# Performance work log

Hardware: AMD Instinct MI355X
Metric: run time of the kernel (lower is better)

Reference implementation:

```python
import jax, jax.numpy as jnp
import numpy as np

N = 100000
F_IN = 128
H = 64
E = 3200000


def setup_inputs() -> dict:
    key = jax.random.key(0)
    ks = jax.random.split(key, 10)
    x = jax.random.normal(ks[0], (N, F_IN), dtype=jnp.float32)
    edge_index = jax.random.randint(ks[1], (2, E), 0, N, dtype=jnp.int64)
    hidden_state = jax.random.normal(ks[2], (1, N, H), dtype=jnp.float32)
    # GCNConv params (glorot-ish scale)
    W_gcn = jax.random.normal(ks[3], (F_IN, H), dtype=jnp.float32) / np.sqrt(F_IN)
    b_gcn = jnp.zeros((H,), dtype=jnp.float32)
    # torch.nn.GRU params, layout [3H, in] with gate order (r, z, n)
    s = 1.0 / np.sqrt(H)
    W_ih = jax.random.uniform(ks[4], (3 * H, H), dtype=jnp.float32, minval=-s, maxval=s)
    W_hh = jax.random.uniform(ks[5], (3 * H, H), dtype=jnp.float32, minval=-s, maxval=s)
    b_ih = jax.random.uniform(ks[6], (3 * H,), dtype=jnp.float32, minval=-s, maxval=s)
    b_hh = jax.random.uniform(ks[7], (3 * H,), dtype=jnp.float32, minval=-s, maxval=s)
    return {"x": x, "edge_index": edge_index, "hidden_state": hidden_state,
            "W_gcn": W_gcn, "b_gcn": b_gcn,
            "W_ih": W_ih, "W_hh": W_hh, "b_ih": b_ih, "b_hh": b_hh}


def gcn_conv(x, edge_index, W, b):
    n = x.shape[0]
    # add self-loops (PyG GCNConv default)
    loops = jnp.arange(n, dtype=edge_index.dtype)
    row = jnp.concatenate([edge_index[0], loops])  # source
    col = jnp.concatenate([edge_index[1], loops])  # target
    # symmetric normalization: deg over targets with unit edge weights
    deg = jax.ops.segment_sum(jnp.ones_like(col, dtype=x.dtype), col, num_segments=n)
    dis = jnp.where(deg > 0, jax.lax.rsqrt(deg), 0.0)
    norm = dis[row] * dis[col]  # (E+N,)
    xt = x @ W  # (N, H) transform first, then aggregate
    msg = norm[:, None] * xt[row]  # (E+N, H)
    out = jax.ops.segment_sum(msg, col, num_segments=n)
    return out + b


def gru_step(x, h, W_ih, W_hh, b_ih, b_hh):
    # single-step torch GRU, gate order (r, z, n)
    gi = x @ W_ih.T + b_ih  # (N, 3H)
    gh = h @ W_hh.T + b_hh
    i_r, i_z, i_n = jnp.split(gi, 3, axis=-1)
    h_r, h_z, h_n = jnp.split(gh, 3, axis=-1)
    r = jax.nn.sigmoid(i_r + h_r)
    z = jax.nn.sigmoid(i_z + h_z)
    n = jnp.tanh(i_n + r * h_n)
    return (1.0 - z) * n + z * h


def reference(x, edge_index, hidden_state, W_gcn, b_gcn, W_ih, W_hh, b_ih, b_hh):
    g = jax.nn.relu(gcn_conv(x, edge_index, W_gcn, b_gcn))  # (N, H)
    h_new = gru_step(g, hidden_state[0], W_ih, W_hh, b_ih, b_hh)  # (N, H)
    return h_new, h_new[None]  # (out, new_hidden_state)
```

## Files before the change

kernel.cpp:

```cpp
#include <hip/hip_runtime.h>
#include <cmath>

constexpr int NN  = 100000;
constexpr int FIN = 128;
constexpr int HH  = 64;
constexpr int NE  = 3200000;
constexpr int NB  = (NN + 255) / 256;
constexpr int NFB  = NB;
constexpr int PCAP = 10240;

typedef __attribute__((ext_vector_type(8))) short short8;
typedef __attribute__((ext_vector_type(4))) float f32x4;

__device__ __forceinline__ ushort f2bf(float x) {
    unsigned u = __float_as_uint(x);
    u += 0x7FFF + ((u >> 16) & 1);
    return (ushort)(u >> 16);
}
__device__ __forceinline__ float bf2f(ushort h) {
    return __uint_as_float(((unsigned)h) << 16);
}
__device__ __forceinline__ unsigned pack2(float a, float b) {
    return (unsigned)f2bf(a) | ((unsigned)f2bf(b) << 16);
}

__global__ void __launch_bounds__(256) k_part(const int* __restrict__ ei,
                                              int* __restrict__ gcnt,
                                              int* __restrict__ pairs) {
    __shared__ int lcnt[NFB];
    __shared__ int lbase[NFB];
    int t = threadIdx.x;
    for (int i = t; i < NFB; i += 256) lcnt[i] = 0;
    __syncthreads();

    long long base = (long long)blockIdx.x * 8192;
    int4 r4[8], c4[8];
    int nv[8];
#pragma unroll
    for (int s = 0; s < 8; ++s) {
        long long e = base + s * 1024 + t * 4;
        if (e < NE) {
            r4[s] = ((const int4*)(ei))[e >> 2];
            c4[s] = ((const int4*)(ei + NE))[e >> 2];
            nv[s] = 1;
            atomicAdd(&lcnt[c4[s].x >> 8], 1);
            atomicAdd(&lcnt[c4[s].y >> 8], 1);
            atomicAdd(&lcnt[c4[s].z >> 8], 1);
            atomicAdd(&lcnt[c4[s].w >> 8], 1);
        } else {
            nv[s] = 0;
        }
    }
    __syncthreads();
    for (int i = t; i < NFB; i += 256) {
        int c = lcnt[i];
        lbase[i] = c ? atomicAdd(&gcnt[i], c) : 0;
        lcnt[i] = 0;
    }
    __syncthreads();
#pragma unroll
    for (int s = 0; s < 8; ++s) {
        if (!nv[s]) continue;
        int rr[4] = {r4[s].x, r4[s].y, r4[s].z, r4[s].w};
        int cc[4] = {c4[s].x, c4[s].y, c4[s].z, c4[s].w};
#pragma unroll
        for (int k = 0; k < 4; ++k) {
            int b   = cc[k] >> 8;
            int p   = atomicAdd(&lcnt[b], 1);
            int pos = lbase[b] + p;
            if (pos < PCAP) pairs[(long long)b * PCAP + pos] = (rr[k] << 8) | (cc[k] & 255);
        }
    }
}

__global__ void __launch_bounds__(256) k_csr(const int* __restrict__ pairs,
                                             const int* __restrict__ gcnt,
                                             int* __restrict__ deg,
                                             int* __restrict__ rowptr,
                                             float* __restrict__ dis,
                                             int* __restrict__ csr) {
    __shared__ int sg[256];
    __shared__ int ldeg[256];
    __shared__ int lrp[256];
    __shared__ int lcur[256];
    __shared__ int lcsr[PCAP];
    int f = blockIdx.x;
    int t = threadIdx.x;
    int partial = 0;
    if (t < f) partial += gcnt[t];
    if (t + 256 < f) partial += gcnt[t + 256];
    sg[t] = partial;
    ldeg[t] = 0;
    __syncthreads();
    for (int off = 128; off > 0; off >>= 1) {
        if (t < off) sg[t] += sg[t + off];
        __syncthreads();
    }
    int base = sg[0];
    int cnt  = min(gcnt[f], PCAP);
    int n0   = f * 256;
    const int* pb = pairs + (long long)f * PCAP;
    for (int i = t; i < cnt; i += 256) atomicAdd(&ldeg[pb[i] & 255], 1);
    __syncthreads();
    int v = ldeg[t];
    lrp[t] = v;
    __syncthreads();
    for (int off = 1; off < 256; off <<= 1) {
        int add = (t >= off) ? lrp[t - off] : 0;
        __syncthreads();
        lrp[t] += add;
        __syncthreads();
    }
    int excl = lrp[t] - v;
    if (n0 + t < NN) {
        deg[n0 + t]    = v;
        rowptr[n0 + t] = base + excl;
        dis[n0 + t]    = rsqrtf((float)(v + 1));
    }
    lcur[t] = excl;
    __syncthreads();
    for (int i = t; i < cnt; i += 256) {
        int e = pb[i];
        int p = atomicAdd(&lcur[e & 255], 1);
        lcsr[p] = e >> 8;
    }
    __syncthreads();
    for (int i = t; i < cnt; i += 256) csr[base + i] = lcsr[i];
}

__global__ void __launch_bounds__(256) k_xt(const float* __restrict__ x,
                                            const float* __restrict__ W,
                                            ushort* __restrict__ xtb) {
    __shared__ float part[16 * 256];
    int t    = threadIdx.x;
    int lane = t & 63;
    int kbase = __builtin_amdgcn_readfirstlane((t >> 6) * 32);
    float wreg[32];
#pragma unroll
    for (int kk = 0; kk < 32; ++kk) wreg[kk] = W[(kbase + kk) * HH + lane];

    for (int ph = blockIdx.x; ph < 6250; ph += gridDim.x) {
        int rowBase = ph * 16;
#pragma unroll 2
        for (int r = 0; r < 16; ++r) {
            const float* xr = x + (size_t)(rowBase + r) * FIN + kbase;
            float acc = 0.f;
#pragma unroll
            for (int kk = 0; kk < 32; ++kk) acc = fmaf(xr[kk], wreg[kk], acc);
            part[r * 256 + (kbase << 1) + lane] = acc;
        }
        __syncthreads();
        unsigned* xo = (unsigned*)(xtb + (size_t)rowBase * HH);
        const float2* p2 = (const float2*)part;
#pragma unroll
        for (int rr = 0; rr < 2; ++rr) {
            int u  = t + 256 * rr;
            int r  = u >> 5;
            int cp = u & 31;
            float2 a0 = p2[r * 128 + cp];
            float2 a1 = p2[r * 128 + cp + 32];
            float2 a2 = p2[r * 128 + cp + 64];
            float2 a3 = p2[r * 128 + cp + 96];
            xo[u] = pack2(a0.x + a1.x + a2.x + a3.x, a0.y + a1.y + a2.y + a3.y);
        }
        __syncthreads();
    }
}

__global__ void __launch_bounds__(256) k_gather(const int* __restrict__ csr,
                                                const int* __restrict__ rowptr,
                                                const int* __restrict__ deg,
                                                const float* __restrict__ dis,
                                                const ushort* __restrict__ xtb,
                                                const float* __restrict__ bg,
                                                float* __restrict__ g) {
    __shared__ int   lid[4][64];
    __shared__ float ldi[4][64];
    int t    = threadIdx.x;
    int lane = t & 63;
    int w    = t >> 6;
    int n    = blockIdx.x * 4 + w;
    int r = lane >> 3;
    int q = lane & 7;
    float acc[8] = {0.f, 0.f, 0.f, 0.f, 0.f, 0.f, 0.f, 0.f};
    float dn  = dis[n];
    int start = rowptr[n];
    int cnt   = deg[n];
    for (int c0 = 0; c0 < cnt; c0 += 64) {
        int m = min(64, cnt - c0);
        if (lane < m) {
            int id = csr[start + c0 + lane];
            lid[w][lane] = id;
            ldi[w][lane] = dis[id];
        }
        for (int i = r; i < m; i += 8) {
            int   src = lid[w][i];
            float d   = ldi[w][i];
            short8 v = ((const short8*)(xtb + (size_t)src * HH))[q];
#pragma unroll
            for (int j = 0; j < 8; ++j)
                acc[j] = fmaf(d, bf2f((ushort)v[j]), acc[j]);
        }
    }
#pragma unroll
    for (int j = 0; j < 8; ++j) {
        acc[j] += __shfl_xor(acc[j], 8, 64);
        acc[j] += __shfl_xor(acc[j], 16, 64);
        acc[j] += __shfl_xor(acc[j], 32, 64);
    }
    if (r == 0) {
        short8 xs = ((const short8*)(xtb + (size_t)n * HH))[q];
        float4 b0 = ((const float4*)bg)[q * 2];
        float4 b1 = ((const float4*)bg)[q * 2 + 1];
        float bb[8] = {b0.x, b0.y, b0.z, b0.w, b1.x, b1.y, b1.z, b1.w};
        float res[8];
#pragma unroll
        for (int j = 0; j < 8; ++j)
            res[j] = fmaxf(fmaf(dn, fmaf(dn, bf2f((ushort)xs[j]), acc[j]), bb[j]), 0.f);
        float4* go = (float4*)(g + (size_t)n * HH + q * 8);
        go[0] = make_float4(res[0], res[1], res[2], res[3]);
        go[1] = make_float4(res[4], res[5], res[6], res[7]);
    }
}

__global__ void k_wprep(const float* __restrict__ Wih, const float* __restrict__ Whh,
                        ushort* __restrict__ bsp) {
    ushort* Bhi  = bsp;
    ushort* Blo  = bsp + 192 * 128;
    ushort* BShi = bsp + 2 * 192 * 128;
    ushort* BSlo = BShi + 64 * 64;
    int i = blockIdx.x * 256 + threadIdx.x;
    if (i < 192 * 128) {
        int j = i >> 7, k = i & 127;
        float wv = (k < 64) ? Wih[j * 64 + k] : Whh[j * 64 + (k - 64)];
        ushort hi = f2bf(wv);
        Bhi[i] = hi;
        Blo[i] = f2bf(wv - bf2f(hi));
    }
    if (i < 64 * 64) {
        int j = i >> 6, k = i & 63;
        float wv = Whh[(128 + j) * 64 + k];
        ushort hi = f2bf(wv);
        BShi[i] = hi;
        BSlo[i] = f2bf(wv - bf2f(hi));
    }
}

__global__ void __launch_bounds__(256) k_gru(
    const float* __restrict__ gbuf, const float* __restrict__ hprev,
    const ushort* __restrict__ bsp,
    const float* __restrict__ bih, const float* __restrict__ bhh,
    float* __restrict__ out) {
    __shared__ ushort Ahi[64 * 136];
    __shared__ ushort Alo[64 * 136];
    const ushort* Bhi  = bsp;
    const ushort* Blo  = bsp + 192 * 128;
    const ushort* BShi = bsp + 2 * 192 * 128;
    const ushort* BSlo = BShi + 64 * 64;

    int t  = threadIdx.x;
    int n0 = blockIdx.x * 64;

    unsigned* Ahi32 = (unsigned*)Ahi;
    unsigned* Alo32 = (unsigned*)Alo;
#pragma unroll
    for (int s = 0; s < 4; ++s) {
        int idx = t + 256 * s;
        int nd  = idx >> 4;
        int kq  = idx & 15;
        bool ok = (n0 + nd) < NN;
        float4 vg = ok ? ((const float4*)(gbuf  + (size_t)(n0 + nd) * HH))[kq]
                       : make_float4(0.f, 0.f, 0.f, 0.f);
        float4 vh = ok ? ((const float4*)(hprev + (size_t)(n0 + nd) * HH))[kq]
                       : make_float4(0.f, 0.f, 0.f, 0.f);
        int bg2 = nd * 68 + kq * 2;
        int bh2 = bg2 + 32;
        float ghx = bf2f(f2bf(vg.x)), ghy = bf2f(f2bf(vg.y));
        float ghz = bf2f(f2bf(vg.z)), ghw = bf2f(f2bf(vg.w));
        float hhx = bf2f(f2bf(vh.x)), hhy = bf2f(f2bf(vh.y));
        float hhz = bf2f(f2bf(vh.z)), hhw = bf2f(f2bf(vh.w));
        Ahi32[bg2]     = pack2(vg.x, vg.y);
        Ahi32[bg2 + 1] = pack2(vg.z, vg.w);
        Alo32[bg2]     = pack2(vg.x - ghx, vg.y - ghy);
        Alo32[bg2 + 1] = pack2(vg.z - ghz, vg.w - ghw);
        Ahi32[bh2]     = pack2(vh.x, vh.y);
        Ahi32[bh2 + 1] = pack2(vh.z, vh.w);
        Alo32[bh2]     = pack2(vh.x - hhx, vh.y - hhy);
        Alo32[bh2 + 1] = pack2(vh.z - hhz, vh.w - hhw);
    }
    __syncthreads();

    int lane  = t & 63;
    int w     = t >> 6;
    int l15   = lane & 15;
    int kbase = (lane >> 4) * 8;

    f32x4 acc[4][4];
#pragma unroll
    for (int a = 0; a < 4; ++a)
#pragma unroll
        for (int m = 0; m < 4; ++m) acc[a][m] = (f32x4){0.f, 0.f, 0.f, 0.f};

#pragma unroll
    for (int g = 0; g < 3; ++g) {
        int brow = (w + 4 * g) * 16 + l15;
        short8 bh[4], bl[4];
#pragma unroll
        for (int ks = 0; ks < 4; ++ks) {
            bh[ks] = *(const short8*)(Bhi + brow * 128 + ks * 32 + kbase);
            bl[ks] = *(const short8*)(Blo + brow * 128 + ks * 32 + kbase);
        }
#pragma unroll
        for (int mt = 0; mt < 4; ++mt) {
            int abase = (mt * 16 + l15) * 136 + kbase;
#pragma unroll
            for (int ks = 0; ks < 4; ++ks) {
                short8 ah = *(const short8*)&Ahi[abase + ks * 32];
                short8 al = *(const short8*)&Alo[abase + ks * 32];
                acc[g][mt] = __builtin_amdgcn_mfma_f32_16x16x32_bf16(ah, bh[ks], acc[g][mt], 0, 0, 0);
                acc[g][mt] = __builtin_amdgcn_mfma_f32_16x16x32_bf16(al, bh[ks], acc[g][mt], 0, 0, 0);
                acc[g][mt] = __builtin_amdgcn_mfma_f32_16x16x32_bf16(ah, bl[ks], acc[g][mt], 0, 0, 0);
            }
        }
    }
    {
        int brow = w * 16 + l15;
        short8 bh[2], bl[2];
#pragma unroll
        for (int ks = 0; ks < 2; ++ks) {
            bh[ks] = *(const short8*)(BShi + brow * 64 + ks * 32 + kbase);
            bl[ks] = *(const short8*)(BSlo + brow * 64 + ks * 32 + kbase);
        }
#pragma unroll
        for (int mt = 0; mt < 4; ++mt) {
            int abase = (mt * 16 + l15) * 136 + 64 + kbase;
#pragma unroll
            for (int ks = 0; ks < 2; ++ks) {
                short8 ah = *(const short8*)&Ahi[abase + ks * 32];
                short8 al = *(const short8*)&Alo[abase + ks * 32];
                acc[3][mt] = __builtin_amdgcn_mfma_f32_16x16x32_bf16(ah, bh[ks], acc[3][mt], 0, 0, 0);
                acc[3][mt] = __builtin_amdgcn_mfma_f32_16x16x32_bf16(al, bh[ks], acc[3][mt], 0, 0, 0);
                acc[3][mt] = __builtin_amdgcn_mfma_f32_16x16x32_bf16(ah, bl[ks], acc[3][mt], 0, 0, 0);
            }
        }
    }

    int j = 16 * w + l15;
    float br  = bih[j] + bhh[j];
    float bz  = bih[HH + j] + bhh[HH + j];
    float bin = bih[2 * HH + j];
    float bhn = bhh[2 * HH + j];
#pragma unroll
    for (int mt = 0; mt < 4; ++mt) {
#pragma unroll
        for (int reg = 0; reg < 4; ++reg) {
            int row  = mt * 16 + (lane >> 4) * 4 + reg;
            int node = n0 + row;
            if (node < NN) {
                float S1 = acc[0][mt][reg];
                float S2 = acc[1][mt][reg];
                float S3 = acc[2][mt][reg];
                float Hn = acc[3][mt][reg];
                float r  = __builtin_amdgcn_rcpf(1.f + __expf(-(S1 + br)));
                float z  = __builtin_amdgcn_rcpf(1.f + __expf(-(S2 + bz)));
                float na = (S3 - Hn + bin) + r * (Hn + bhn);
                float e2 = __expf(2.f * na);
                float nv = fmaf(-2.f, __builtin_amdgcn_rcpf(1.f + e2), 1.f);
                int lidx = row * 136 + 64 + j;
                float h  = bf2f(Ahi[lidx]) + bf2f(Alo[lidx]);
                float o  = (1.f - z) * nv + z * h;
                out[(size_t)node * HH + j] = o;
                out[(size_t)NN * HH + (size_t)node * HH + j] = o;
            }
        }
    }
}

extern "C" void kernel_launch(void* const* d_in, const int* in_sizes, int n_in,
                              void* d_out, int out_size, void* d_ws, size_t ws_size,
                              hipStream_t stream) {
    const float* x   = (const float*)d_in[0];
    const int*   ei  = (const int*)d_in[1];
    const float* hs  = (const float*)d_in[2];
    const float* Wg  = (const float*)d_in[3];
    const float* bg  = (const float*)d_in[4];
    const float* Wih = (const float*)d_in[5];
    const float* Whh = (const float*)d_in[6];
    const float* bih = (const float*)d_in[7];
    const float* bhh = (const float*)d_in[8];
    float* out = (float*)d_out;

    char* ws = (char*)d_ws;
    int*    pairs  = (int*)   (ws);
    ushort* xtb    = (ushort*)(ws);
    float*  gbuf   = (float*) (ws + 16400000);
    int*    csr    = (int*)   (ws + 42000000);
    int*    deg    = (int*)   (ws + 54800000);
    int*    rowptr = (int*)   (ws + 55200000);
    float*  dis    = (float*) (ws + 55600000);
    ushort* wsplit = (ushort*)(ws + 56000000);
    int*    gcnt   = (int*)   (ws + 56200000);

    hipMemsetAsync(gcnt, 0, NFB * sizeof(int), stream);

    hipLaunchKernelGGL(k_wprep, dim3(96), dim3(256), 0, stream, Wih, Whh, wsplit);
    hipLaunchKernelGGL(k_part,  dim3((NE + 8191) / 8192), dim3(256), 0, stream, ei, gcnt, pairs);
    hipLaunchKernelGGL(k_csr,   dim3(NFB), dim3(256), 0, stream,
                       pairs, gcnt, deg, rowptr, dis, csr);
    hipLaunchKernelGGL(k_xt,    dim3(1024), dim3(256), 0, stream, x, Wg, xtb);
    hipLaunchKernelGGL(k_gather, dim3(NN / 4), dim3(256), 0, stream,
                       csr, rowptr, deg, dis, xtb, bg, gbuf);
    hipLaunchKernelGGL(k_gru,   dim3((NN + 63) / 64), dim3(256), 0, stream,
                       gbuf, hs, wsplit, bih, bhh, out);
}
```

Measured before the change: 365.1 us.

## Pre-scale transformed features by dis and simplify gather; retune partition and CSR kernels

Folds the source-side degree normalization into the feature transform, so each row of the bf16 xt buffer is already multiplied by dis[src]. This removes the per-edge dis gather and the multiply from the aggregation kernel, which is now unrolled by two to keep more loads in flight. The partition kernel also handles smaller chunks per block, giving more blocks, and the CSR build kernel runs with 512 threads. A small change in bf16 rounding comes from scaling before quantization.

```diff
diff --git a/kernel.cpp b/kernel.cpp
--- a/kernel.cpp
+++ b/kernel.cpp
@@ -8,6 +8,7 @@
 constexpr int NB  = (NN + 255) / 256;
 constexpr int NFB  = NB;
 constexpr int PCAP = 10240;
+constexpr int CH   = 2048;
 
 typedef __attribute__((ext_vector_type(8))) short short8;
 typedef __attribute__((ext_vector_type(4))) float f32x4;
@@ -33,12 +34,12 @@
     for (int i = t; i < NFB; i += 256) lcnt[i] = 0;
     __syncthreads();
 
-    long long base = (long long)blockIdx.x * 8192;
-    int4 r4[8], c4[8];
-    int nv[8];
-#pragma unroll
-    for (int s = 0; s < 8; ++s) {
-        long long e = base + s * 1024 + t * 4;
+    int base = blockIdx.x * CH;
+    int4 r4[2], c4[2];
+    int nv[2];
+#pragma unroll
+    for (int s = 0; s < 2; ++s) {
+        int e = base + s * 1024 + t * 4;
         if (e < NE) {
             r4[s] = ((const int4*)(ei))[e >> 2];
             c4[s] = ((const int4*)(ei + NE))[e >> 2];
@@ -59,7 +60,7 @@
     }
     __syncthreads();
 #pragma unroll
-    for (int s = 0; s < 8; ++s) {
+    for (int s = 0; s < 2; ++s) {
         if (!nv[s]) continue;
         int rr[4] = {r4[s].x, r4[s].y, r4[s].z, r4[s].w};
         int cc[4] = {c4[s].x, c4[s].y, c4[s].z, c4[s].w};
@@ -68,41 +69,38 @@
             int b   = cc[k] >> 8;
             int p   = atomicAdd(&lcnt[b], 1);
             int pos = lbase[b] + p;
-            if (pos < PCAP) pairs[(long long)b * PCAP + pos] = (rr[k] << 8) | (cc[k] & 255);
-        }
-    }
-}
-
-__global__ void __launch_bounds__(256) k_csr(const int* __restrict__ pairs,
+            if (pos < PCAP) pairs[b * PCAP + pos] = (rr[k] << 8) | (cc[k] & 255);
+        }
+    }
+}
+
+__global__ void __launch_bounds__(512) k_csr(const int* __restrict__ pairs,
                                              const int* __restrict__ gcnt,
                                              int* __restrict__ deg,
                                              int* __restrict__ rowptr,
                                              float* __restrict__ dis,
                                              int* __restrict__ csr) {
-    __shared__ int sg[256];
+    __shared__ int sg[512];
     __shared__ int ldeg[256];
-    __shared__ int lrp[256];
+    __shared__ int lrp[512];
     __shared__ int lcur[256];
     __shared__ int lcsr[PCAP];
     int f = blockIdx.x;
     int t = threadIdx.x;
-    int partial = 0;
-    if (t < f) partial += gcnt[t];
-    if (t + 256 < f) partial += gcnt[t + 256];
-    sg[t] = partial;
-    ldeg[t] = 0;
-    __syncthreads();
-    for (int off = 128; off > 0; off >>= 1) {
+    sg[t] = (t < f) ? gcnt[t] : 0;
+    if (t < 256) ldeg[t] = 0;
+    __syncthreads();
+    for (int off = 256; off > 0; off >>= 1) {
         if (t < off) sg[t] += sg[t + off];
         __syncthreads();
     }
     int base = sg[0];
     int cnt  = min(gcnt[f], PCAP);
     int n0   = f * 256;
-    const int* pb = pairs + (long long)f * PCAP;
-    for (int i = t; i < cnt; i += 256) atomicAdd(&ldeg[pb[i] & 255], 1);
-    __syncthreads();
-    int v = ldeg[t];
+    const int* pb = pairs + f * PCAP;
+    for (int i = t; i < cnt; i += 512) atomicAdd(&ldeg[pb[i] & 255], 1);
+    __syncthreads();
+    int v = (t < 256) ? ldeg[t] : 0;
     lrp[t] = v;
     __syncthreads();
     for (int off = 1; off < 256; off <<= 1) {
@@ -112,24 +110,27 @@
         __syncthreads();
     }
     int excl = lrp[t] - v;
-    if (n0 + t < NN) {
-        deg[n0 + t]    = v;
-        rowptr[n0 + t] = base + excl;
-        dis[n0 + t]    = rsqrtf((float)(v + 1));
-    }
-    lcur[t] = excl;
-    __syncthreads();
-    for (int i = t; i < cnt; i += 256) {
+    if (t < 256) {
+        if (n0 + t < NN) {
+            deg[n0 + t]    = v;
+            rowptr[n0 + t] = base + excl;
+            dis[n0 + t]    = rsqrtf((float)(v + 1));
+        }
+        lcur[t] = excl;
+    }
+    __syncthreads();
+    for (int i = t; i < cnt; i += 512) {
         int e = pb[i];
         int p = atomicAdd(&lcur[e & 255], 1);
         lcsr[p] = e >> 8;
     }
     __syncthreads();
-    for (int i = t; i < cnt; i += 256) csr[base + i] = lcsr[i];
+    for (int i = t; i < cnt; i += 512) csr[base + i] = lcsr[i];
 }
 
 __global__ void __launch_bounds__(256) k_xt(const float* __restrict__ x,
                                             const float* __restrict__ W,
+                                            const float* __restrict__ dis,
                                             ushort* __restrict__ xtb) {
     __shared__ float part[16 * 256];
     int t    = threadIdx.x;
@@ -157,11 +158,13 @@
             int u  = t + 256 * rr;
             int r  = u >> 5;
             int cp = u & 31;
+            float ds = dis[rowBase + r];
             float2 a0 = p2[r * 128 + cp];
             float2 a1 = p2[r * 128 + cp + 32];
             float2 a2 = p2[r * 128 + cp + 64];
             float2 a3 = p2[r * 128 + cp + 96];
-            xo[u] = pack2(a0.x + a1.x + a2.x + a3.x, a0.y + a1.y + a2.y + a3.y);
+            xo[u] = pack2(ds * (a0.x + a1.x + a2.x + a3.x),
+                          ds * (a0.y + a1.y + a2.y + a3.y));
         }
         __syncthreads();
     }
@@ -174,8 +177,7 @@
                                                 const ushort* __restrict__ xtb,
                                                 const float* __restrict__ bg,
                                                 float* __restrict__ g) {
-    __shared__ int   lid[4][64];
-    __shared__ float ldi[4][64];
+    __shared__ int lid[4][64];
     int t    = threadIdx.x;
     int lane = t & 63;
     int w    = t >> 6;
@@ -188,18 +190,23 @@
     int cnt   = deg[n];
     for (int c0 = 0; c0 < cnt; c0 += 64) {
         int m = min(64, cnt - c0);
-        if (lane < m) {
-            int id = csr[start + c0 + lane];
-            lid[w][lane] = id;
-            ldi[w][lane] = dis[id];
-        }
-        for (int i = r; i < m; i += 8) {
-            int   src = lid[w][i];
-            float d   = ldi[w][i];
-            short8 v = ((const short8*)(xtb + (size_t)src * HH))[q];
-#pragma unroll
-            for (int j = 0; j < 8; ++j)
-                acc[j] = fmaf(d, bf2f((ushort)v[j]), acc[j]);
+        if (lane < m) lid[w][lane] = csr[start + c0 + lane];
+        int i = r;
+        for (; i + 8 < m; i += 16) {
+            int s0 = lid[w][i];
+            int s1 = lid[w][i + 8];
+            short8 v0 = ((const short8*)(xtb + (size_t)s0 * HH))[q];
+            short8 v1 = ((const short8*)(xtb + (size_t)s1 * HH))[q];
+#pragma unroll
+            for (int j = 0; j < 8; ++j) acc[j] += bf2f((ushort)v0[j]);
+#pragma unroll
+            for (int j = 0; j < 8; ++j) acc[j] += bf2f((ushort)v1[j]);
+        }
+        if (i < m) {
+            int s0 = lid[w][i];
+            short8 v0 = ((const short8*)(xtb + (size_t)s0 * HH))[q];
+#pragma unroll
+            for (int j = 0; j < 8; ++j) acc[j] += bf2f((ushort)v0[j]);
         }
     }
 #pragma unroll
@@ -216,7 +223,7 @@
         float res[8];
 #pragma unroll
         for (int j = 0; j < 8; ++j)
-            res[j] = fmaxf(fmaf(dn, fmaf(dn, bf2f((ushort)xs[j]), acc[j]), bb[j]), 0.f);
+            res[j] = fmaxf(fmaf(dn, acc[j] + bf2f((ushort)xs[j]), bb[j]), 0.f);
         float4* go = (float4*)(g + (size_t)n * HH + q * 8);
         go[0] = make_float4(res[0], res[1], res[2], res[3]);
         go[1] = make_float4(res[4], res[5], res[6], res[7]);
@@ -404,10 +411,10 @@
     hipMemsetAsync(gcnt, 0, NFB * sizeof(int), stream);
 
     hipLaunchKernelGGL(k_wprep, dim3(96), dim3(256), 0, stream, Wih, Whh, wsplit);
-    hipLaunchKernelGGL(k_part,  dim3((NE + 8191) / 8192), dim3(256), 0, stream, ei, gcnt, pairs);
-    hipLaunchKernelGGL(k_csr,   dim3(NFB), dim3(256), 0, stream,
+    hipLaunchKernelGGL(k_part,  dim3((NE + CH - 1) / CH), dim3(256), 0, stream, ei, gcnt, pairs);
+    hipLaunchKernelGGL(k_csr,   dim3(NFB), dim3(512), 0, stream,
                        pairs, gcnt, deg, rowptr, dis, csr);
-    hipLaunchKernelGGL(k_xt,    dim3(1024), dim3(256), 0, stream, x, Wg, xtb);
+    hipLaunchKernelGGL(k_xt,    dim3(1024), dim3(256), 0, stream, x, Wg, dis, xtb);
     hipLaunchKernelGGL(k_gather, dim3(NN / 4), dim3(256), 0, stream,
                        csr, rowptr, deg, dis, xtb, bg, gbuf);
     hipLaunchKernelGGL(k_gru,   dim3((NN + 63) / 64), dim3(256), 0, stream,
```

New measurement: 392.9 us. 1.08x slower.

## Compute x@W with split-bf16 MFMA and fold source normalization into xt

Applied to the files above, without the earlier changes.

The dense feature transform moves from scalar FMA with an LDS reduction to bf16 MFMA, using a hi/lo split of both x and W_gcn (three MFMAs per step) to stay close to fp32 accuracy. The split weight is prepared in the existing weight-prep kernel. Each output row is pre-scaled by its source dis before being stored as bf16, so the gather no longer loads dis per neighbour and just sums rows, now unrolled two at a time. The risk is extra rounding from scaling before the bf16 store; the pair offsets also drop their 64-bit casts.

```diff
diff --git a/kernel.cpp b/kernel.cpp
--- a/kernel.cpp
+++ b/kernel.cpp
@@ -68,7 +68,7 @@
             int b   = cc[k] >> 8;
             int p   = atomicAdd(&lcnt[b], 1);
             int pos = lbase[b] + p;
-            if (pos < PCAP) pairs[(long long)b * PCAP + pos] = (rr[k] << 8) | (cc[k] & 255);
+            if (pos < PCAP) pairs[b * PCAP + pos] = (rr[k] << 8) | (cc[k] & 255);
         }
     }
 }
@@ -99,7 +99,7 @@
     int base = sg[0];
     int cnt  = min(gcnt[f], PCAP);
     int n0   = f * 256;
-    const int* pb = pairs + (long long)f * PCAP;
+    const int* pb = pairs + f * PCAP;
     for (int i = t; i < cnt; i += 256) atomicAdd(&ldeg[pb[i] & 255], 1);
     __syncthreads();
     int v = ldeg[t];
@@ -129,41 +129,78 @@
 }
 
 __global__ void __launch_bounds__(256) k_xt(const float* __restrict__ x,
-                                            const float* __restrict__ W,
+                                            const ushort* __restrict__ wgx,
+                                            const float* __restrict__ dis,
                                             ushort* __restrict__ xtb) {
-    __shared__ float part[16 * 256];
-    int t    = threadIdx.x;
-    int lane = t & 63;
-    int kbase = __builtin_amdgcn_readfirstlane((t >> 6) * 32);
-    float wreg[32];
-#pragma unroll
-    for (int kk = 0; kk < 32; ++kk) wreg[kk] = W[(kbase + kk) * HH + lane];
-
-    for (int ph = blockIdx.x; ph < 6250; ph += gridDim.x) {
-        int rowBase = ph * 16;
-#pragma unroll 2
-        for (int r = 0; r < 16; ++r) {
-            const float* xr = x + (size_t)(rowBase + r) * FIN + kbase;
-            float acc = 0.f;
-#pragma unroll
-            for (int kk = 0; kk < 32; ++kk) acc = fmaf(xr[kk], wreg[kk], acc);
-            part[r * 256 + (kbase << 1) + lane] = acc;
-        }
-        __syncthreads();
-        unsigned* xo = (unsigned*)(xtb + (size_t)rowBase * HH);
-        const float2* p2 = (const float2*)part;
-#pragma unroll
-        for (int rr = 0; rr < 2; ++rr) {
-            int u  = t + 256 * rr;
-            int r  = u >> 5;
-            int cp = u & 31;
-            float2 a0 = p2[r * 128 + cp];
-            float2 a1 = p2[r * 128 + cp + 32];
-            float2 a2 = p2[r * 128 + cp + 64];
-            float2 a3 = p2[r * 128 + cp + 96];
-            xo[u] = pack2(a0.x + a1.x + a2.x + a3.x, a0.y + a1.y + a2.y + a3.y);
-        }
-        __syncthreads();
+    __shared__ ushort Ahi[64 * 136];
+    __shared__ ushort Alo[64 * 136];
+    __shared__ float sdis[64];
+    const ushort* GXhi = wgx;
+    const ushort* GXlo = wgx + 64 * 128;
+    int t  = threadIdx.x;
+    int r0 = blockIdx.x * 64;
+    if (t < 64) sdis[t] = (r0 + t < NN) ? dis[r0 + t] : 0.f;
+    unsigned* Ahi32 = (unsigned*)Ahi;
+    unsigned* Alo32 = (unsigned*)Alo;
+#pragma unroll
+    for (int s = 0; s < 8; ++s) {
+        int idx = t + 256 * s;
+        int nd  = idx >> 5;
+        int kq  = idx & 31;
+        bool ok = (r0 + nd) < NN;
+        float4 v = ok ? ((const float4*)(x + (size_t)(r0 + nd) * FIN))[kq]
+                      : make_float4(0.f, 0.f, 0.f, 0.f);
+        int b2 = nd * 68 + kq * 2;
+        float hx = bf2f(f2bf(v.x)), hy = bf2f(f2bf(v.y));
+        float hz = bf2f(f2bf(v.z)), hw = bf2f(f2bf(v.w));
+        Ahi32[b2]     = pack2(v.x, v.y);
+        Ahi32[b2 + 1] = pack2(v.z, v.w);
+        Alo32[b2]     = pack2(v.x - hx, v.y - hy);
+        Alo32[b2 + 1] = pack2(v.z - hz, v.w - hw);
+    }
+    __syncthreads();
+
+    int lane = t & 63, w = t >> 6, l15 = lane & 15;
+    int kbase = (lane >> 4) * 8;
+    int j = w * 16 + l15;
+    f32x4 acc[4];
+#pragma unroll
+    for (int m = 0; m < 4; ++m) acc[m] = (f32x4){0.f, 0.f, 0.f, 0.f};
+    short8 bh[4], bl[4];
+#pragma unroll
+    for (int ks = 0; ks < 4; ++ks) {
+        bh[ks] = *(const short8*)(GXhi + j * 128 + ks * 32 + kbase);
+        bl[ks] = *(const short8*)(GXlo + j * 128 + ks * 32 + kbase);
+    }
+#pragma unroll
+    for (int mt = 0; mt < 4; ++mt) {
+        int abase = (mt * 16 + l15) * 136 + kbase;
+#pragma unroll
+        for (int ks = 0; ks < 4; ++ks) {
+            short8 ah = *(const short8*)&Ahi[abase + ks * 32];
+            short8 al = *(const short8*)&Alo[abase + ks * 32];
+            acc[mt] = __builtin_amdgcn_mfma_f32_16x16x32_bf16(ah, bh[ks], acc[mt], 0, 0, 0);
+            acc[mt] = __builtin_amdgcn_mfma_f32_16x16x32_bf16(al, bh[ks], acc[mt], 0, 0, 0);
+            acc[mt] = __builtin_amdgcn_mfma_f32_16x16x32_bf16(ah, bl[ks], acc[mt], 0, 0, 0);
+        }
+    }
+    __syncthreads();
+#pragma unroll
+    for (int mt = 0; mt < 4; ++mt) {
+#pragma unroll
+        for (int reg = 0; reg < 4; ++reg) {
+            int row = mt * 16 + (lane >> 4) * 4 + reg;
+            Alo[row * 64 + j] = f2bf(sdis[row] * acc[mt][reg]);
+        }
+    }
+    __syncthreads();
+    const uint4* src = (const uint4*)Alo;
+    uint4* dst = (uint4*)(xtb + (size_t)r0 * HH);
+#pragma unroll
+    for (int s = 0; s < 2; ++s) {
+        int u   = t + 256 * s;
+        int row = u >> 3;
+        if (r0 + row < NN) dst[u] = src[u];
     }
 }
 
@@ -174,8 +211,7 @@
                                                 const ushort* __restrict__ xtb,
                                                 const float* __restrict__ bg,
                                                 float* __restrict__ g) {
-    __shared__ int   lid[4][64];
-    __shared__ float ldi[4][64];
+    __shared__ int lid[4][64];
     int t    = threadIdx.x;
     int lane = t & 63;
     int w    = t >> 6;
@@ -188,18 +224,23 @@
     int cnt   = deg[n];
     for (int c0 = 0; c0 < cnt; c0 += 64) {
         int m = min(64, cnt - c0);
-        if (lane < m) {
-            int id = csr[start + c0 + lane];
-            lid[w][lane] = id;
-            ldi[w][lane] = dis[id];
-        }
-        for (int i = r; i < m; i += 8) {
-            int   src = lid[w][i];
-            float d   = ldi[w][i];
-            short8 v = ((const short8*)(xtb + (size_t)src * HH))[q];
-#pragma unroll
-            for (int j = 0; j < 8; ++j)
-                acc[j] = fmaf(d, bf2f((ushort)v[j]), acc[j]);
+        if (lane < m) lid[w][lane] = csr[start + c0 + lane];
+        int i = r;
+        for (; i + 8 < m; i += 16) {
+            int s0 = lid[w][i];
+            int s1 = lid[w][i + 8];
+            short8 v0 = ((const short8*)(xtb + (size_t)s0 * HH))[q];
+            short8 v1 = ((const short8*)(xtb + (size_t)s1 * HH))[q];
+#pragma unroll
+            for (int j = 0; j < 8; ++j) acc[j] += bf2f((ushort)v0[j]);
+#pragma unroll
+            for (int j = 0; j < 8; ++j) acc[j] += bf2f((ushort)v1[j]);
+        }
+        if (i < m) {
+            int s0 = lid[w][i];
+            short8 v0 = ((const short8*)(xtb + (size_t)s0 * HH))[q];
+#pragma unroll
+            for (int j = 0; j < 8; ++j) acc[j] += bf2f((ushort)v0[j]);
         }
     }
 #pragma unroll
@@ -216,7 +257,7 @@
         float res[8];
 #pragma unroll
         for (int j = 0; j < 8; ++j)
-            res[j] = fmaxf(fmaf(dn, fmaf(dn, bf2f((ushort)xs[j]), acc[j]), bb[j]), 0.f);
+            res[j] = fmaxf(fmaf(dn, acc[j] + bf2f((ushort)xs[j]), bb[j]), 0.f);
         float4* go = (float4*)(g + (size_t)n * HH + q * 8);
         go[0] = make_float4(res[0], res[1], res[2], res[3]);
         go[1] = make_float4(res[4], res[5], res[6], res[7]);
@@ -224,11 +265,13 @@
 }
 
 __global__ void k_wprep(const float* __restrict__ Wih, const float* __restrict__ Whh,
-                        ushort* __restrict__ bsp) {
+                        const float* __restrict__ Wg, ushort* __restrict__ bsp) {
     ushort* Bhi  = bsp;
     ushort* Blo  = bsp + 192 * 128;
     ushort* BShi = bsp + 2 * 192 * 128;
     ushort* BSlo = BShi + 64 * 64;
+    ushort* GXhi = BSlo + 64 * 64;
+    ushort* GXlo = GXhi + 64 * 128;
     int i = blockIdx.x * 256 + threadIdx.x;
     if (i < 192 * 128) {
         int j = i >> 7, k = i & 127;
@@ -243,6 +286,13 @@
         ushort hi = f2bf(wv);
         BShi[i] = hi;
         BSlo[i] = f2bf(wv - bf2f(hi));
+    }
+    if (i < 64 * 128) {
+        int j = i >> 7, k = i & 127;
+        float wv = Wg[k * HH + j];
+        ushort hi = f2bf(wv);
+        GXhi[i] = hi;
+        GXlo[i] = f2bf(wv - bf2f(hi));
     }
 }
 
@@ -403,11 +453,12 @@
 
     hipMemsetAsync(gcnt, 0, NFB * sizeof(int), stream);
 
-    hipLaunchKernelGGL(k_wprep, dim3(96), dim3(256), 0, stream, Wih, Whh, wsplit);
+    hipLaunchKernelGGL(k_wprep, dim3(96), dim3(256), 0, stream, Wih, Whh, Wg, wsplit);
     hipLaunchKernelGGL(k_part,  dim3((NE + 8191) / 8192), dim3(256), 0, stream, ei, gcnt, pairs);
     hipLaunchKernelGGL(k_csr,   dim3(NFB), dim3(256), 0, stream,
                        pairs, gcnt, deg, rowptr, dis, csr);
-    hipLaunchKernelGGL(k_xt,    dim3(1024), dim3(256), 0, stream, x, Wg, xtb);
+    hipLaunchKernelGGL(k_xt,    dim3((NN + 63) / 64), dim3(256), 0, stream,
+                       x, wsplit + 2 * 192 * 128 + 2 * 64 * 64, dis, xtb);
     hipLaunchKernelGGL(k_gather, dim3(NN / 4), dim3(256), 0, stream,
                        csr, rowptr, deg, dis, xtb, bg, gbuf);
     hipLaunchKernelGGL(k_gru,   dim3((NN + 63) / 64), dim3(256), 0, stream,
```

Measured after the change: 318.1 us. -12.9%, faster.
